# Kernel optimization log

Measured on AMD Instinct MI355X. Metric: run time of the kernel, lower is better.

The kernel has to match this reference:

```python
import jax, jax.numpy as jnp
import numpy as np

P_DIM = 128
NV = 33000; NP_ = 33000; ND = 33000
N = NV + NP_ + ND            # 99000 nodes
E = 800000                    # edges
G = 64                        # graphs in batch
R = 4                         # message-passing iterations


def setup_inputs() -> dict:
    key = jax.random.key(0)
    ks = jax.random.split(key, 24)
    f = lambda k, s: jax.random.normal(k, s, dtype=jnp.float32)
    w = lambda k, s: 0.05 * jax.random.normal(k, s, dtype=jnp.float32)
    inp = {
        "edge_attr": f(ks[0], (E,)),
        "node_mu": f(ks[1], (N, P_DIM)),
        "x_vehicle": f(ks[2], (NV, 2)),
        "x_pickup": f(ks[3], (NP_, 3)),
        "x_dropoff": f(ks[4], (ND, 2)),
        # torch Linear weights stored as (in, out); y = x @ W + b
        "W1": w(ks[5], (P_DIM, P_DIM)), "b1": w(ks[6], (P_DIM,)),
        "W2": w(ks[7], (P_DIM, P_DIM)), "b2": w(ks[8], (P_DIM,)),
        "W3": w(ks[9], (1, P_DIM)),     "b3": w(ks[10], (P_DIM,)),
        "Wv": w(ks[11], (2, P_DIM)),    "bv": w(ks[12], (P_DIM,)),
        "Wp": w(ks[13], (3, P_DIM)),    "bp": w(ks[14], (P_DIM,)),
        "Wd": w(ks[15], (2, P_DIM)),    "bd": w(ks[16], (P_DIM,)),
        "Wc": w(ks[17], (P_DIM, 1)),    "bc": w(ks[18], (1,)),
        "edge_index": jax.random.randint(ks[19], (2, E), 0, N),
        # block layout: first NV vehicles (type 0), then pickups (1), dropoffs (2)
        "node_types": jnp.concatenate([
            jnp.zeros((NV,), jnp.int32),
            jnp.ones((NP_,), jnp.int32),
            jnp.full((ND,), 2, jnp.int32)]),
        "batch": jnp.sort(jax.random.randint(ks[20], (N,), 0, G)),
        "num_graphs": G,
    }
    return inp


def reference(edge_attr, node_mu, x_vehicle, x_pickup, x_dropoff,
              W1, b1, W2, b2, W3, b3, Wv, bv, Wp, bp, Wd, bd, Wc, bc,
              edge_index, node_types, batch, num_graphs):
    n_nodes = node_mu.shape[0]
    src, dst = edge_index[0], edge_index[1]

    # theta3 on edge attrs (constant across iterations -> hoisted, same math)
    t = jax.nn.leaky_relu(edge_attr[:, None] @ W3 + b3)          # (E, p)
    agg_t = jax.ops.segment_sum(t, dst, num_segments=n_nodes)    # (N, p)
    t_term = agg_t @ W2 + b2                                     # theta2 term

    # per-node-type additive transform; node types are laid out in blocks so
    # mu[mask] += Linear_t(x_t) is a block-ordered concat (constant per iter)
    type_add = jnp.concatenate([
        x_vehicle @ Wv + bv,
        x_pickup @ Wp + bp,
        x_dropoff @ Wd + bd], axis=0)                            # (N, p)

    mu = node_mu
    for _ in range(R):
        agg_mu = jax.ops.segment_sum(mu[src], dst, num_segments=n_nodes)
        mu = jax.nn.leaky_relu(agg_mu @ W1 + b1 + t_term + type_add)

    # scatter_mean over graph ids
    g_sum = jax.ops.segment_sum(mu, batch, num_segments=num_graphs)
    counts = jax.ops.segment_sum(jnp.ones((n_nodes,), mu.dtype), batch,
                                 num_segments=num_graphs)
    g = g_sum / jnp.maximum(counts, 1.0)[:, None]                # (G, p)
    proba = jax.nn.sigmoid(g @ Wc + bc)                          # (G, 1)
    return proba
```

## Files before the change

kernel.cpp:

```cpp
#include <hip/hip_runtime.h>
#include <math.h>

#define P 128

typedef __attribute__((ext_vector_type(8))) short short8;
typedef __attribute__((ext_vector_type(4))) float f32x4;

static __device__ __forceinline__ float lrelu(float x){ return x > 0.f ? x : 0.01f*x; }
static __device__ __forceinline__ float bflo(unsigned u){ union{unsigned u; float f;} c; c.u = u << 16; return c.f; }
static __device__ __forceinline__ float bfhi(unsigned u){ union{unsigned u; float f;} c; c.u = u & 0xffff0000u; return c.f; }
static __device__ __forceinline__ unsigned fbits(float f){ union{float f; unsigned u;} c; c.f = f; return c.u; }
static __device__ __forceinline__ unsigned packbf(float x, float y){
  unsigned ux = fbits(x); ux += 0x7fffu + ((ux >> 16) & 1u);
  unsigned uy = fbits(y); uy += 0x7fffu + ((uy >> 16) & 1u);
  return (ux >> 16) | (uy & 0xffff0000u);
}

__global__ void k_hist(const int* __restrict__ dst, int E, int* __restrict__ cnt){
  for(int i = blockIdx.x*blockDim.x + threadIdx.x; i < E; i += gridDim.x*blockDim.x)
    atomicAdd(&cnt[dst[i]], 1);
}

__global__ void k_scan1(const int* __restrict__ cnt, int N, int* __restrict__ off, int* __restrict__ partial){
  __shared__ int s[256];
  int t = threadIdx.x, i = blockIdx.x*256 + t;
  int v = (i < N) ? cnt[i] : 0;
  s[t] = v; __syncthreads();
  for(int o = 1; o < 256; o <<= 1){
    int x = (t >= o) ? s[t-o] : 0; __syncthreads();
    s[t] += x; __syncthreads();
  }
  if(i < N) off[i] = s[t];
  if(t == 255) partial[blockIdx.x] = s[255];
}

__global__ void k_scan2(int* __restrict__ partial, int nb){
  __shared__ int s[512];
  int t = threadIdx.x;
  int v = (t < nb) ? partial[t] : 0;
  s[t] = v; __syncthreads();
  for(int o = 1; o < 512; o <<= 1){
    int x = (t >= o) ? s[t-o] : 0; __syncthreads();
    s[t] += x; __syncthreads();
  }
  if(t < nb) partial[t] = s[t] - v;
}

__global__ void k_scan3(const int* __restrict__ cnt, int N, int E, int* __restrict__ off, const int* __restrict__ partial){
  int i = blockIdx.x*256 + threadIdx.x;
  if(i < N) off[i] = off[i] - cnt[i] + partial[blockIdx.x];
  if(i == 0) off[N] = E;
}

__global__ void k_scatter(const int* __restrict__ ei, const float* __restrict__ ea, int E,
                          const int* __restrict__ off, int* __restrict__ cur,
                          int* __restrict__ csr_src, float* __restrict__ csr_attr){
  const int* src = ei; const int* dst = ei + E;
  for(int i = blockIdx.x*blockDim.x + threadIdx.x; i < E; i += gridDim.x*blockDim.x){
    int d = dst[i];
    int p = off[d] + atomicAdd(&cur[d], 1);
    csr_src[p]  = src[i];
    csr_attr[p] = ea[i];
  }
}

__global__ void k_cvt(const float2* __restrict__ in, unsigned* __restrict__ out, int n){
  int i = blockIdx.x*256 + threadIdx.x;
  if(i < n){ float2 v = in[i]; out[i] = packbf(v.x, v.y); }
}

__global__ void k_wprep(const float* __restrict__ W1, const float* __restrict__ W2,
                        unsigned* __restrict__ W1T, unsigned* __restrict__ W2T,
                        const float* __restrict__ Wv, const float* __restrict__ bv,
                        const float* __restrict__ Wp, const float* __restrict__ bp,
                        const float* __restrict__ Wd, const float* __restrict__ bd,
                        const float* __restrict__ b1, const float* __restrict__ b2,
                        unsigned* __restrict__ W2Tx){
  int b = blockIdx.x, t = threadIdx.x;
  if(b < 256){
    if(t < 64){
      const float* W = (b < 128) ? W1 : W2;
      unsigned* WT   = (b < 128) ? W1T : W2T;
      int j = b & 127, k2 = t;
      float a = W[(size_t)(2*k2)*P + j], c = W[(size_t)(2*k2+1)*P + j];
      WT[(size_t)j*64 + k2] = packbf(a, c);
    }
  } else {
    int j = t;
    unsigned q[16];
    #pragma unroll
    for(int i = 0; i < 16; ++i) q[i] = 0;
    q[0] = packbf(Wv[j],     Wv[128+j]);
    q[1] = packbf(Wp[j],     Wp[128+j]);
    q[2] = packbf(Wp[256+j], Wd[j]);
    q[3] = packbf(Wd[128+j], b1[j] + b2[j]);
    q[4] = packbf(bv[j],     bp[j]);
    q[5] = packbf(bd[j],     0.f);
    uint4* dst = (uint4*)(W2Tx + (size_t)j*16);
    #pragma unroll
    for(int i = 0; i < 4; ++i) dst[i] = make_uint4(q[4*i], q[4*i+1], q[4*i+2], q[4*i+3]);
  }
}

__global__ __launch_bounds__(512) void k_gemmB(
    const int* __restrict__ off, const float* __restrict__ csr_attr,
    const float* __restrict__ W3, const float* __restrict__ b3,
    const short8* __restrict__ WT, const short8* __restrict__ WTx,
    const float* __restrict__ xv, const float* __restrict__ xp, const float* __restrict__ xd,
    int NV, int NP_, int N, unsigned* __restrict__ Out){
  __shared__ __align__(16) unsigned shu[5376];
  int t = threadIdx.x, w = t >> 6, l = t & 63;
  int bm = blockIdx.x * 64;

  {
    float w0 = W3[2*l], w1 = W3[2*l+1];
    float c0 = b3[2*l], c1 = b3[2*l+1];
    for(int i = 0; i < 8; ++i){
      int row = w*8 + i, node = bm + row;
      float a0=0.f, a1=0.f, g0=0.f, g1=0.f;
      if(node < N){
        int s0 = off[node], s1 = off[node+1];
        int p = s0;
        for(; p+3 < s1; p += 4){
          float e0 = csr_attr[p], e1 = csr_attr[p+1], e2 = csr_attr[p+2], e3 = csr_attr[p+3];
          a0 += lrelu(fmaf(e0, w0, c0)); a1 += lrelu(fmaf(e0, w1, c1));
          g0 += lrelu(fmaf(e1, w0, c0)); g1 += lrelu(fmaf(e1, w1, c1));
          a0 += lrelu(fmaf(e2, w0, c0)); a1 += lrelu(fmaf(e2, w1, c1));
          g0 += lrelu(fmaf(e3, w0, c0)); g1 += lrelu(fmaf(e3, w1, c1));
        }
        for(; p < s1; ++p){
          float e = csr_attr[p];
          a0 += lrelu(fmaf(e, w0, c0)); a1 += lrelu(fmaf(e, w1, c1));
        }
      }
      shu[(row*256 + ((l*4) ^ ((row&7)<<4))) >> 2] = packbf(a0+g0, a1+g1);
    }
  }
  {
    int r = t >> 3, q = t & 7;
    int node = bm + r;
    float x0=0.f, x1=0.f, x2=0.f; int ty = 3;
    if(node < N){
      if(node < NV){ ty = 0; x0 = xv[2*node]; x1 = xv[2*node+1]; }
      else if(node < NV + NP_){ int i2 = node - NV; ty = 1; x0 = xp[3*i2]; x1 = xp[3*i2+1]; x2 = xp[3*i2+2]; }
      else { int i2 = node - NV - NP_; ty = 2; x0 = xd[2*i2]; x1 = xd[2*i2+1]; }
    }
    float s0v, s1v;
    switch(q){
      case 0: s0v = (ty==0)?x0:0.f; s1v = (ty==0)?x1:0.f; break;
      case 1: s0v = (ty==1)?x0:0.f; s1v = (ty==1)?x1:0.f; break;
      case 2: s0v = (ty==1)?x2:0.f; s1v = (ty==2)?x0:0.f; break;
      case 3: s0v = (ty==2)?x1:0.f; s1v = (node<N)?1.f:0.f; break;
      case 4: s0v = (ty==0)?1.f:0.f; s1v = (ty==1)?1.f:0.f; break;
      case 5: s0v = (ty==2)?1.f:0.f; s1v = 0.f; break;
      default: s0v = 0.f; s1v = 0.f; break;
    }
    shu[4096 + r*20 + q]     = packbf(s0v, s1v);
    shu[4096 + r*20 + 8 + q] = 0u;
  }
  __syncthreads();

  int lr = l & 15, lg = l >> 4;
  int wm = w & 3, wn = w >> 2;
  f32x4 acc[4];
  #pragma unroll
  for(int i = 0; i < 4; ++i) acc[i] = (f32x4)0.f;
  int arow = wm*16 + lr;
  #pragma unroll
  for(int ks = 0; ks < 4; ++ks){
    short8 a = *(const short8*)((const char*)shu + arow*256 + ((((ks*4+lg)*16) ^ ((arow&7)<<4))));
    #pragma unroll
    for(int ct = 0; ct < 4; ++ct){
      short8 b = WT[(size_t)(wn*64 + ct*16 + lr)*16 + ks*4 + lg];
      acc[ct] = __builtin_amdgcn_mfma_f32_16x16x32_bf16(a, b, acc[ct], 0, 0, 0);
    }
  }
  {
    short8 a = *(const short8*)&shu[4096 + arow*20 + lg*4];
    #pragma unroll
    for(int ct = 0; ct < 4; ++ct){
      short8 b = WTx[(size_t)(wn*64 + ct*16 + lr)*4 + lg];
      acc[ct] = __builtin_amdgcn_mfma_f32_16x16x32_bf16(a, b, acc[ct], 0, 0, 0);
    }
  }
  __syncthreads();

  float* shf = (float*)shu;
  int r = t >> 3, seg = t & 7;
  int row = bm + r;
  #pragma unroll
  for(int h = 0; h < 2; ++h){
    if(wn == h){
      #pragma unroll
      for(int ct = 0; ct < 4; ++ct)
        #pragma unroll
        for(int rr = 0; rr < 4; ++rr)
          shf[(wm*16 + lg*4 + rr)*68 + ct*16 + lr] = acc[ct][rr];
    }
    __syncthreads();
    if(row < N){
      float4 v0 = *(const float4*)&shf[r*68 + seg*8];
      float4 v1 = *(const float4*)&shf[r*68 + seg*8 + 4];
      *(uint4*)&Out[(size_t)row*64 + h*32 + seg*4] =
        make_uint4(packbf(v0.x,v0.y), packbf(v0.z,v0.w), packbf(v1.x,v1.y), packbf(v1.z,v1.w));
    }
    __syncthreads();
  }
}

__global__ __launch_bounds__(512) void k_fused(
    const int* __restrict__ off, const int* __restrict__ csr_src,
    const unsigned* __restrict__ mu, const short8* __restrict__ WT,
    const unsigned* __restrict__ baseB, unsigned* __restrict__ Out, int N){
  __shared__ __align__(16) float shf[64*68];
  __shared__ int sbound[8][9];
  int t = threadIdx.x, w = t >> 6, l = t & 63;
  int bm = blockIdx.x * 64;
  unsigned* Albs = (unsigned*)shf;

  if(l < 9) sbound[w][l] = off[min(bm + w*8 + l, N)];

  {
    int e0   = sbound[w][0];
    int eEnd = sbound[w][8];
    int cur = 0;
    int nb = sbound[w][1];
    float ax = 0.f, ay = 0.f;
    int e = e0;
    for(; e + 16 <= eEnd; e += 16){
      unsigned v[16];
      #pragma unroll
      for(int k = 0; k < 16; ++k){
        int idx = csr_src[e + k];
        v[k] = mu[(size_t)idx*64 + l];
      }
      #pragma unroll
      for(int k = 0; k < 16; ++k){
        while(e + k >= nb){
          Albs[((w*8+cur)*256 + ((l*4) ^ (((w*8+cur)&7)<<4))) >> 2] = packbf(ax, ay);
          ax = 0.f; ay = 0.f; ++cur; nb = sbound[w][cur + 1];
        }
        ax += bflo(v[k]); ay += bfhi(v[k]);
      }
    }
    if(e < eEnd){
      unsigned v[16];
      #pragma unroll
      for(int k = 0; k < 16; ++k){
        int idx = csr_src[min(e + k, eEnd - 1)];
        v[k] = mu[(size_t)idx*64 + l];
      }
      #pragma unroll
      for(int k = 0; k < 16; ++k){
        if(e + k >= eEnd) break;
        while(e + k >= nb){
          Albs[((w*8+cur)*256 + ((l*4) ^ (((w*8+cur)&7)<<4))) >> 2] = packbf(ax, ay);
          ax = 0.f; ay = 0.f; ++cur; nb = sbound[w][cur + 1];
        }
        ax += bflo(v[k]); ay += bfhi(v[k]);
      }
    }
    for(; cur < 8; ++cur){
      Albs[((w*8+cur)*256 + ((l*4) ^ (((w*8+cur)&7)<<4))) >> 2] = packbf(ax, ay);
      ax = 0.f; ay = 0.f;
    }
  }
  __syncthreads();

  int lr = l & 15, lg = l >> 4;
  int wm = w & 3, wn = w >> 2;
  f32x4 acc[4];
  #pragma unroll
  for(int i = 0; i < 4; ++i) acc[i] = (f32x4)0.f;
  int arow = wm*16 + lr;
  #pragma unroll
  for(int ks = 0; ks < 4; ++ks){
    short8 a = *(const short8*)((const char*)shf + arow*256 + ((((ks*4+lg)*16) ^ ((arow&7)<<4))));
    #pragma unroll
    for(int ct = 0; ct < 4; ++ct){
      short8 b = WT[(size_t)(wn*64 + ct*16 + lr)*16 + ks*4 + lg];
      acc[ct] = __builtin_amdgcn_mfma_f32_16x16x32_bf16(a, b, acc[ct], 0, 0, 0);
    }
  }
  __syncthreads();

  int r = t >> 3, seg = t & 7;
  int row = bm + r;
  #pragma unroll
  for(int h = 0; h < 2; ++h){
    if(wn == h){
      #pragma unroll
      for(int ct = 0; ct < 4; ++ct)
        #pragma unroll
        for(int rr = 0; rr < 4; ++rr)
          shf[(wm*16 + lg*4 + rr)*68 + ct*16 + lr] = acc[ct][rr];
    }
    __syncthreads();
    if(row < N){
      float4 v0 = *(const float4*)&shf[r*68 + seg*8];
      float4 v1 = *(const float4*)&shf[r*68 + seg*8 + 4];
      const unsigned* ad = baseB + (size_t)row*64 + h*32 + seg*4;
      unsigned b0 = ad[0], b1u = ad[1], b2u = ad[2], b3u = ad[3];
      *(uint4*)&Out[(size_t)row*64 + h*32 + seg*4] = make_uint4(
        packbf(lrelu(v0.x + bflo(b0)),  lrelu(v0.y + bfhi(b0))),
        packbf(lrelu(v0.z + bflo(b1u)), lrelu(v0.w + bfhi(b1u))),
        packbf(lrelu(v1.x + bflo(b2u)), lrelu(v1.y + bfhi(b2u))),
        packbf(lrelu(v1.z + bflo(b3u)), lrelu(v1.w + bfhi(b3u))));
    }
    __syncthreads();
  }
}

#define GSB 256
__global__ void k_gsum(const unsigned* __restrict__ mu, const int* __restrict__ batch, int N,
                       float* __restrict__ gsum){
  int c = threadIdx.x & 63, sub = threadIdx.x >> 6;
  int n0 = blockIdx.x * GSB;
  int n1 = min(n0 + GSB, N);
  float ax = 0.f, ay = 0.f; int curg = -1;
  for(int n = n0 + sub; n < n1; n += 4){
    int g = batch[n];
    if(g != curg){
      if(curg >= 0){ atomicAdd(&gsum[curg*P + 2*c], ax); atomicAdd(&gsum[curg*P + 2*c + 1], ay); }
      curg = g; ax = 0.f; ay = 0.f;
    }
    unsigned v = mu[(size_t)n*64 + c];
    ax += bflo(v); ay += bfhi(v);
  }
  if(curg >= 0){ atomicAdd(&gsum[curg*P + 2*c], ax); atomicAdd(&gsum[curg*P + 2*c + 1], ay); }
}

__global__ void k_out(const float* __restrict__ gsum, const int* __restrict__ batch, int N,
                      const float* __restrict__ Wc, const float* __restrict__ bc,
                      float* __restrict__ out){
  int g = blockIdx.x, t = threadIdx.x;
  int lo = 0, hi = N;
  while(lo < hi){ int m=(lo+hi)>>1; if(batch[m] < g) lo = m+1; else hi = m; }
  int start = lo; lo = start; hi = N;
  while(lo < hi){ int m=(lo+hi)>>1; if(batch[m] <= g) lo = m+1; else hi = m; }
  int cnt = lo - start;
  float cf = cnt < 1 ? 1.f : (float)cnt;
  __shared__ float red[128];
  red[t] = (gsum[g*P + t] / cf) * Wc[t];
  __syncthreads();
  for(int o = 64; o > 0; o >>= 1){ if(t < o) red[t] += red[t+o]; __syncthreads(); }
  if(t == 0) out[g] = 1.f/(1.f + expf(-(red[0] + bc[0])));
}

extern "C" void kernel_launch(void* const* d_in, const int* in_sizes, int n_in,
                              void* d_out, int out_size, void* d_ws, size_t ws_size,
                              hipStream_t stream){
  const float* edge_attr = (const float*)d_in[0];
  const float* node_mu   = (const float*)d_in[1];
  const float* xv = (const float*)d_in[2];
  const float* xp = (const float*)d_in[3];
  const float* xd = (const float*)d_in[4];
  const float* W1 = (const float*)d_in[5];  const float* b1 = (const float*)d_in[6];
  const float* W2 = (const float*)d_in[7];  const float* b2 = (const float*)d_in[8];
  const float* W3 = (const float*)d_in[9];  const float* b3 = (const float*)d_in[10];
  const float* Wv = (const float*)d_in[11]; const float* bv = (const float*)d_in[12];
  const float* Wp = (const float*)d_in[13]; const float* bp = (const float*)d_in[14];
  const float* Wd = (const float*)d_in[15]; const float* bd = (const float*)d_in[16];
  const float* Wc = (const float*)d_in[17]; const float* bc = (const float*)d_in[18];
  const int*   ei    = (const int*)d_in[19];
  const int*   batch = (const int*)d_in[21];
  const int E   = in_sizes[0];
  const int N   = in_sizes[1] / P;
  const int NV  = in_sizes[2] / 2;
  const int NP_ = in_sizes[3] / 3;
  const int G   = 64;
  float* out = (float*)d_out;

  char* w = (char*)d_ws; size_t o = 0;
  auto alloc = [&](size_t bytes)->void*{ size_t a = (o + 255) & ~(size_t)255; o = a + bytes; return (void*)(w + a); };
  int*      cntcur   = (int*)     alloc((size_t)2*N*4);
  int*      off      = (int*)     alloc((size_t)(N+1)*4);
  int*      partial  = (int*)     alloc(512*4);
  int*      csr_src  = (int*)     alloc((size_t)E*4);
  float*    csr_attr = (float*)   alloc((size_t)E*4);
  unsigned* mu0      = (unsigned*)alloc((size_t)N*64*4);
  unsigned* YA       = (unsigned*)alloc((size_t)N*64*4);
  unsigned* YB       = (unsigned*)alloc((size_t)N*64*4);
  unsigned* baseB    = (unsigned*)alloc((size_t)N*64*4);
  unsigned* W1T      = (unsigned*)alloc((size_t)P*64*4);
  unsigned* W2T      = (unsigned*)alloc((size_t)P*64*4);
  unsigned* W2Tx     = (unsigned*)alloc((size_t)P*16*4);
  float*    gsum     = (float*)   alloc((size_t)G*P*4);
  int* cnt = cntcur; int* cur = cntcur + N;

  hipMemsetAsync(cntcur, 0, (size_t)2*N*4, stream);
  hipMemsetAsync(gsum,   0, (size_t)G*P*4, stream);

  int nb = (N + 255) / 256;
  k_hist   <<<2048, 256, 0, stream>>>(ei + E, E, cnt);
  k_scan1  <<<nb,   256, 0, stream>>>(cnt, N, off, partial);
  k_scan2  <<<1,    512, 0, stream>>>(partial, nb);
  k_scan3  <<<nb,   256, 0, stream>>>(cnt, N, E, off, partial);
  k_scatter<<<2048, 256, 0, stream>>>(ei, edge_attr, E, off, cur, csr_src, csr_attr);

  int nhalf = N*64;
  k_cvt  <<<(nhalf + 255)/256, 256, 0, stream>>>((const float2*)node_mu, mu0, nhalf);
  k_wprep<<<257, 128, 0, stream>>>(W1, W2, W1T, W2T, Wv, bv, Wp, bp, Wd, bd, b1, b2, W2Tx);

  int ggemm = (N + 63) / 64;
  k_gemmB<<<ggemm, 512, 0, stream>>>(off, csr_attr, W3, b3,
                                     (const short8*)W2T, (const short8*)W2Tx,
                                     xv, xp, xd, NV, NP_, N, baseB);

  k_fused<<<ggemm, 512, 0, stream>>>(off, csr_src, mu0, (const short8*)W1T, baseB, YA, N);
  k_fused<<<ggemm, 512, 0, stream>>>(off, csr_src, YA,  (const short8*)W1T, baseB, YB, N);
  k_fused<<<ggemm, 512, 0, stream>>>(off, csr_src, YB,  (const short8*)W1T, baseB, YA, N);
  k_fused<<<ggemm, 512, 0, stream>>>(off, csr_src, YA,  (const short8*)W1T, baseB, YB, N);

  k_gsum<<<(N + GSB - 1)/GSB, 256, 0, stream>>>(YB, batch, N, gsum);
  k_out <<<G, P, 0, stream>>>(gsum, batch, N, Wc, bc, out);
}
```

Measured before the change: 572.4 us.

## Double-buffer CSR gathers and vectorize histogram/scatter edge loads

The fused aggregation kernel and the edge-attribute reduction in k_gemmB now use a two-buffer software pipeline. The next 16-edge batch of gathers is issued before the current one is accumulated, so memory latency can overlap with the adds. k_gemmB also switches from a per-node loop to a warp-wide edge stream with boundary flushes, as k_fused already does. k_hist and k_scatter read edges four at a time with int4/float4 loads and use one thread per four edges instead of a grid-stride loop. The cost is higher register use from the 32-entry buffers, which may lower occupancy. The vector loads also assume E is divisible by 4 for alignment of the dst pointer (ei+E).

```diff
diff --git a/kernel.cpp b/kernel.cpp
--- a/kernel.cpp
+++ b/kernel.cpp
@@ -17,8 +17,15 @@
 }
 
 __global__ void k_hist(const int* __restrict__ dst, int E, int* __restrict__ cnt){
-  for(int i = blockIdx.x*blockDim.x + threadIdx.x; i < E; i += gridDim.x*blockDim.x)
-    atomicAdd(&cnt[dst[i]], 1);
+  int i = blockIdx.x*blockDim.x + threadIdx.x;
+  int i4 = i*4;
+  if(i4 + 4 <= E){
+    int4 d = *(const int4*)(dst + i4);
+    atomicAdd(&cnt[d.x], 1); atomicAdd(&cnt[d.y], 1);
+    atomicAdd(&cnt[d.z], 1); atomicAdd(&cnt[d.w], 1);
+  } else {
+    for(int j = i4; j < E; ++j) atomicAdd(&cnt[dst[j]], 1);
+  }
 }
 
 __global__ void k_scan1(const int* __restrict__ cnt, int N, int* __restrict__ off, int* __restrict__ partial){
@@ -56,11 +63,26 @@
                           const int* __restrict__ off, int* __restrict__ cur,
                           int* __restrict__ csr_src, float* __restrict__ csr_attr){
   const int* src = ei; const int* dst = ei + E;
-  for(int i = blockIdx.x*blockDim.x + threadIdx.x; i < E; i += gridDim.x*blockDim.x){
-    int d = dst[i];
-    int p = off[d] + atomicAdd(&cur[d], 1);
-    csr_src[p]  = src[i];
-    csr_attr[p] = ea[i];
+  int i = blockIdx.x*blockDim.x + threadIdx.x;
+  int i4 = i*4;
+  if(i4 + 4 <= E){
+    int4   s = *(const int4*)(src + i4);
+    int4   d = *(const int4*)(dst + i4);
+    float4 a = *(const float4*)(ea + i4);
+    int p0 = off[d.x] + atomicAdd(&cur[d.x], 1);
+    int p1 = off[d.y] + atomicAdd(&cur[d.y], 1);
+    int p2 = off[d.z] + atomicAdd(&cur[d.z], 1);
+    int p3 = off[d.w] + atomicAdd(&cur[d.w], 1);
+    csr_src[p0] = s.x; csr_attr[p0] = a.x;
+    csr_src[p1] = s.y; csr_attr[p1] = a.y;
+    csr_src[p2] = s.z; csr_attr[p2] = a.z;
+    csr_src[p3] = s.w; csr_attr[p3] = a.w;
+  } else {
+    for(int j = i4; j < E; ++j){
+      int d = dst[j];
+      int p = off[d] + atomicAdd(&cur[d], 1);
+      csr_src[p] = src[j]; csr_attr[p] = ea[j];
+    }
   }
 }
 
@@ -109,31 +131,64 @@
     const float* __restrict__ xv, const float* __restrict__ xp, const float* __restrict__ xd,
     int NV, int NP_, int N, unsigned* __restrict__ Out){
   __shared__ __align__(16) unsigned shu[5376];
+  __shared__ int sbound[8][9];
   int t = threadIdx.x, w = t >> 6, l = t & 63;
   int bm = blockIdx.x * 64;
+
+  if(l < 9) sbound[w][l] = off[min(bm + w*8 + l, N)];
 
   {
     float w0 = W3[2*l], w1 = W3[2*l+1];
     float c0 = b3[2*l], c1 = b3[2*l+1];
-    for(int i = 0; i < 8; ++i){
-      int row = w*8 + i, node = bm + row;
-      float a0=0.f, a1=0.f, g0=0.f, g1=0.f;
-      if(node < N){
-        int s0 = off[node], s1 = off[node+1];
-        int p = s0;
-        for(; p+3 < s1; p += 4){
-          float e0 = csr_attr[p], e1 = csr_attr[p+1], e2 = csr_attr[p+2], e3 = csr_attr[p+3];
-          a0 += lrelu(fmaf(e0, w0, c0)); a1 += lrelu(fmaf(e0, w1, c1));
-          g0 += lrelu(fmaf(e1, w0, c0)); g1 += lrelu(fmaf(e1, w1, c1));
-          a0 += lrelu(fmaf(e2, w0, c0)); a1 += lrelu(fmaf(e2, w1, c1));
-          g0 += lrelu(fmaf(e3, w0, c0)); g1 += lrelu(fmaf(e3, w1, c1));
-        }
-        for(; p < s1; ++p){
-          float e = csr_attr[p];
-          a0 += lrelu(fmaf(e, w0, c0)); a1 += lrelu(fmaf(e, w1, c1));
-        }
-      }
-      shu[(row*256 + ((l*4) ^ ((row&7)<<4))) >> 2] = packbf(a0+g0, a1+g1);
+    int e0 = sbound[w][0], eEnd = sbound[w][8];
+    int cur = 0, nb = sbound[w][1];
+    float ax = 0.f, ay = 0.f;
+    auto flushTo = [&](int edge){
+      while(edge >= nb){
+        int row = w*8 + cur;
+        shu[(row*256 + ((l*4) ^ ((row&7)<<4))) >> 2] = packbf(ax, ay);
+        ax = 0.f; ay = 0.f; ++cur; nb = sbound[w][cur + 1];
+      }
+    };
+    auto loadb = [&](float (&buf)[16], int ebase){
+      #pragma unroll
+      for(int k = 0; k < 16; ++k) buf[k] = csr_attr[ebase + k];
+    };
+    auto procb = [&](float (&buf)[16], int ebase){
+      #pragma unroll
+      for(int k = 0; k < 16; ++k){
+        flushTo(ebase + k);
+        ax += lrelu(fmaf(buf[k], w0, c0));
+        ay += lrelu(fmaf(buf[k], w1, c1));
+      }
+    };
+    int nfull = (eEnd - e0) >> 4;
+    float va[16], vb[16];
+    int b = 0;
+    if(nfull > 0) loadb(va, e0);
+    for(; b + 2 <= nfull; b += 2){
+      loadb(vb, e0 + (b+1)*16);
+      procb(va, e0 + b*16);
+      if(b + 2 < nfull) loadb(va, e0 + (b+2)*16);
+      procb(vb, e0 + (b+1)*16);
+    }
+    if(b < nfull) procb(va, e0 + b*16);
+    int e = e0 + nfull*16;
+    if(e < eEnd){
+      #pragma unroll
+      for(int k = 0; k < 16; ++k) va[k] = csr_attr[min(e + k, eEnd - 1)];
+      #pragma unroll
+      for(int k = 0; k < 16; ++k){
+        if(e + k >= eEnd) break;
+        flushTo(e + k);
+        ax += lrelu(fmaf(va[k], w0, c0));
+        ay += lrelu(fmaf(va[k], w1, c1));
+      }
+    }
+    for(; cur < 8; ++cur){
+      int row = w*8 + cur;
+      shu[(row*256 + ((l*4) ^ ((row&7)<<4))) >> 2] = packbf(ax, ay);
+      ax = 0.f; ay = 0.f;
     }
   }
   {
@@ -226,42 +281,55 @@
     int cur = 0;
     int nb = sbound[w][1];
     float ax = 0.f, ay = 0.f;
-    int e = e0;
-    for(; e + 16 <= eEnd; e += 16){
-      unsigned v[16];
-      #pragma unroll
-      for(int k = 0; k < 16; ++k){
-        int idx = csr_src[e + k];
-        v[k] = mu[(size_t)idx*64 + l];
-      }
-      #pragma unroll
-      for(int k = 0; k < 16; ++k){
-        while(e + k >= nb){
-          Albs[((w*8+cur)*256 + ((l*4) ^ (((w*8+cur)&7)<<4))) >> 2] = packbf(ax, ay);
-          ax = 0.f; ay = 0.f; ++cur; nb = sbound[w][cur + 1];
-        }
-        ax += bflo(v[k]); ay += bfhi(v[k]);
-      }
-    }
+    auto flushTo = [&](int edge){
+      while(edge >= nb){
+        int row = w*8 + cur;
+        Albs[(row*256 + ((l*4) ^ ((row&7)<<4))) >> 2] = packbf(ax, ay);
+        ax = 0.f; ay = 0.f; ++cur; nb = sbound[w][cur + 1];
+      }
+    };
+    auto loadb = [&](unsigned (&buf)[16], int ebase){
+      #pragma unroll
+      for(int k = 0; k < 16; ++k){
+        int idx = csr_src[ebase + k];
+        buf[k] = mu[(size_t)idx*64 + l];
+      }
+    };
+    auto procb = [&](unsigned (&buf)[16], int ebase){
+      #pragma unroll
+      for(int k = 0; k < 16; ++k){
+        flushTo(ebase + k);
+        ax += bflo(buf[k]); ay += bfhi(buf[k]);
+      }
+    };
+    int nfull = (eEnd - e0) >> 4;
+    unsigned va[16], vb[16];
+    int b = 0;
+    if(nfull > 0) loadb(va, e0);
+    for(; b + 2 <= nfull; b += 2){
+      loadb(vb, e0 + (b+1)*16);
+      procb(va, e0 + b*16);
+      if(b + 2 < nfull) loadb(va, e0 + (b+2)*16);
+      procb(vb, e0 + (b+1)*16);
+    }
+    if(b < nfull) procb(va, e0 + b*16);
+    int e = e0 + nfull*16;
     if(e < eEnd){
-      unsigned v[16];
       #pragma unroll
       for(int k = 0; k < 16; ++k){
         int idx = csr_src[min(e + k, eEnd - 1)];
-        v[k] = mu[(size_t)idx*64 + l];
+        va[k] = mu[(size_t)idx*64 + l];
       }
       #pragma unroll
       for(int k = 0; k < 16; ++k){
         if(e + k >= eEnd) break;
-        while(e + k >= nb){
-          Albs[((w*8+cur)*256 + ((l*4) ^ (((w*8+cur)&7)<<4))) >> 2] = packbf(ax, ay);
-          ax = 0.f; ay = 0.f; ++cur; nb = sbound[w][cur + 1];
-        }
-        ax += bflo(v[k]); ay += bfhi(v[k]);
+        flushTo(e + k);
+        ax += bflo(va[k]); ay += bfhi(va[k]);
       }
     }
     for(; cur < 8; ++cur){
-      Albs[((w*8+cur)*256 + ((l*4) ^ (((w*8+cur)&7)<<4))) >> 2] = packbf(ax, ay);
+      int row = w*8 + cur;
+      Albs[(row*256 + ((l*4) ^ ((row&7)<<4))) >> 2] = packbf(ax, ay);
       ax = 0.f; ay = 0.f;
     }
   }
@@ -392,11 +460,12 @@
   hipMemsetAsync(gsum,   0, (size_t)G*P*4, stream);
 
   int nb = (N + 255) / 256;
-  k_hist   <<<2048, 256, 0, stream>>>(ei + E, E, cnt);
+  int ge4 = (E/4 + 255) / 256;
+  k_hist   <<<ge4,  256, 0, stream>>>(ei + E, E, cnt);
   k_scan1  <<<nb,   256, 0, stream>>>(cnt, N, off, partial);
   k_scan2  <<<1,    512, 0, stream>>>(partial, nb);
   k_scan3  <<<nb,   256, 0, stream>>>(cnt, N, E, off, partial);
-  k_scatter<<<2048, 256, 0, stream>>>(ei, edge_attr, E, off, cur, csr_src, csr_attr);
+  k_scatter<<<ge4,  256, 0, stream>>>(ei, edge_attr, E, off, cur, csr_src, csr_attr);
 
   int nhalf = N*64;
   k_cvt  <<<(nhalf + 255)/256, 256, 0, stream>>>((const float2*)node_mu, mu0, nhalf);
```

Result: no change. 579.2 us (+1.2%).
